# Optimization experiments

Hardware: AMD Instinct MI355X
Metric: run time of the kernel (lower is better)

## Reference

```python
import jax, jax.numpy as jnp
import numpy as np

B, D_IN, N_EXP, D_EXP, TOP_K = 8192, 1024, 8, 1024, 2


def setup_inputs() -> dict:
    key = jax.random.key(0)
    ks = jax.random.split(key, 6)
    s_in = 1.0 / np.sqrt(D_IN)
    s_exp = 1.0 / np.sqrt(D_EXP)
    return {
        "x": jax.random.normal(ks[0], (B, D_IN), jnp.float32),
        "gate_w": jax.random.normal(ks[1], (D_IN, N_EXP), jnp.float32) * s_in,
        "w1": jax.random.normal(ks[2], (N_EXP, D_IN, D_EXP), jnp.float32) * s_in,
        "b1": jax.random.normal(ks[3], (N_EXP, D_EXP), jnp.float32) * 0.01,
        "w2": jax.random.normal(ks[4], (N_EXP, D_EXP, D_EXP), jnp.float32) * s_exp,
        "b2": jax.random.normal(ks[5], (N_EXP, D_EXP), jnp.float32) * 0.01,
    }


def _moe(x, gate_w, w1, b1, w2, b2):
    # Gating: top-k sparse softmax over expert logits.
    gate_logits = x @ gate_w                          # (B, E)
    top_vals, top_idx = jax.lax.top_k(gate_logits, TOP_K)  # (B, K)
    # softmax over only the top-k logits == softmax of -inf-scattered logits
    top_w = jax.nn.softmax(top_vals, axis=-1)          # (B, K)
    gate_weights = jnp.zeros_like(gate_logits).at[
        jnp.arange(x.shape[0])[:, None], top_idx
    ].set(top_w)                                       # (B, E)
    # Dense all-expert MLP (matches torch.stack over experts).
    h = jax.nn.gelu(jnp.einsum("bd,edf->ebf", x, w1) + b1[:, None, :],
                    approximate=False)                 # (E, B, F)
    expert_outs = jnp.einsum("ebf,efg->ebg", h, w2) + b2[:, None, :]  # (E, B, G)
    output = jnp.einsum("be,ebg->bg", gate_weights, expert_outs)      # (B, G)
    return output, gate_weights


def reference(x, gate_w, w1, b1, w2, b2):
    return _moe(x, gate_w, w1, b1, w2, b2)
```

## Files before the change

kernel.cpp:

```cpp
#include <hip/hip_runtime.h>
#include <math.h>
#include <stdint.h>


#define NTOK   8192
#define DIN    1024
#define NEXP   8
#define DEXP   1024
#define MAXROWS 17408
#define MAXTILES 136

typedef __bf16 bf16x8_t __attribute__((ext_vector_type(8)));
typedef float f32x4 __attribute__((ext_vector_type(4)));

__device__ __forceinline__ unsigned short f2bf(float f) {
  union { float f; unsigned int u; } v; v.f = f;
  unsigned int u = v.u;
  u += 0x7fffu + ((u >> 16) & 1u);
  return (unsigned short)(u >> 16);
}

__device__ __forceinline__ float bf2f(unsigned short s) {
  union { unsigned int u; float f; } v; v.u = ((unsigned int)s) << 16;
  return v.f;
}

__device__ __forceinline__ void async16(const void* g, void* l) {
  __builtin_amdgcn_global_load_lds((const __attribute__((address_space(1))) void*)g,
                                   (__attribute__((address_space(3))) void*)l, 16, 0, 0);
}

__device__ __forceinline__ float gelu_fast(float v) {
  float u = v * (1.5957691216057308f + 0.07135481627f * v * v);
  return v * (1.0f / (1.0f + __expf(-u)));
}

__global__ __launch_bounds__(256) void prep_kernel(const float* __restrict__ x,
                                                   const float* __restrict__ gw,
                                                   const float* __restrict__ w1,
                                                   const float* __restrict__ w2,
                                                   unsigned short* __restrict__ xbf,
                                                   unsigned short* __restrict__ w1T,
                                                   unsigned short* __restrict__ w2T,
                                                   float* __restrict__ outGate,
                                                   int* __restrict__ topE,
                                                   float* __restrict__ topW,
                                                   int* __restrict__ rowTok) {
  __shared__ float tile[64][68];
  int b = blockIdx.x;
  int tid = threadIdx.x;
  if (b < 4096) {
    int z = b >> 8;
    const float* src = (z < 8) ? w1 : w2;
    unsigned short* dst = (z < 8) ? w1T : w2T;
    int e = z & 7;
    int idx = b & 255, kt = idx >> 4, nt = idx & 15;
    const float* s = src + (size_t)e * DIN * DEXP + (size_t)kt * 64 * 1024 + nt * 64;
    unsigned short* d = dst + (size_t)e * DIN * DEXP + (size_t)nt * 64 * 1024 + kt * 64;
    int c4 = (tid & 15) * 4, r0 = tid >> 4;
    #pragma unroll
    for (int p = 0; p < 4; ++p) {
      int r = r0 + p * 16;
      *(float4*)&tile[r][c4] = *(const float4*)(s + (size_t)r * 1024 + c4);
    }
    __syncthreads();
    #pragma unroll
    for (int p = 0; p < 4; ++p) {
      int nr = r0 + p * 16;
      ushort4 o;
      o.x = f2bf(tile[c4 + 0][nr]);
      o.y = f2bf(tile[c4 + 1][nr]);
      o.z = f2bf(tile[c4 + 2][nr]);
      o.w = f2bf(tile[c4 + 3][nr]);
      *(ushort4*)(d + (size_t)nr * 1024 + c4) = o;
    }
  } else if (b < 6144) {
    int lane = tid & 63, wv = tid >> 6;
    int t = (b - 4096) * 4 + wv;
    const float4* xr = (const float4*)(x + (size_t)t * 1024);
    ushort4* xo = (ushort4*)(xbf + (size_t)t * 1024);
    double acc[NEXP];
    #pragma unroll
    for (int e = 0; e < NEXP; ++e) acc[e] = 0.0;
    #pragma unroll
    for (int j = 0; j < 4; ++j) {
      int q = lane + 64 * j;
      float4 v = xr[q];
      ushort4 r;
      r.x = f2bf(v.x); r.y = f2bf(v.y); r.z = f2bf(v.z); r.w = f2bf(v.w);
      xo[q] = r;
      float vv[4] = {v.x, v.y, v.z, v.w};
      #pragma unroll
      for (int m = 0; m < 4; ++m) {
        int k = q * 4 + m;
        float4 g0 = *(const float4*)(gw + k * 8);
        float4 g1 = *(const float4*)(gw + k * 8 + 4);
        double xv = (double)vv[m];
        acc[0] += xv * (double)g0.x; acc[1] += xv * (double)g0.y;
        acc[2] += xv * (double)g0.z; acc[3] += xv * (double)g0.w;
        acc[4] += xv * (double)g1.x; acc[5] += xv * (double)g1.y;
        acc[6] += xv * (double)g1.z; acc[7] += xv * (double)g1.w;
      }
    }
    #pragma unroll
    for (int off = 32; off > 0; off >>= 1) {
      #pragma unroll
      for (int e = 0; e < NEXP; ++e) acc[e] += __shfl_xor(acc[e], off);
    }
    if (lane == 0) {
      int e0 = 0; double v0 = acc[0];
      #pragma unroll
      for (int e = 1; e < NEXP; ++e) if (acc[e] > v0) { v0 = acc[e]; e0 = e; }
      int e1 = -1; double v1 = -1e300;
      #pragma unroll
      for (int e = 0; e < NEXP; ++e) if (e != e0 && acc[e] > v1) { v1 = acc[e]; e1 = e; }
      float ex = expf((float)(v1 - v0));
      float inv = 1.0f / (1.0f + ex);
      float w0 = inv, w1v = ex * inv;
      float g8[8];
      #pragma unroll
      for (int e = 0; e < NEXP; ++e) g8[e] = 0.f;
      g8[e0] = w0; g8[e1] = w1v;
      float4* gp = (float4*)(outGate + t * 8);
      gp[0] = *(float4*)&g8[0];
      gp[1] = *(float4*)&g8[4];
      topE[t * 2 + 0] = e0; topE[t * 2 + 1] = e1;
      topW[t * 2 + 0] = w0; topW[t * 2 + 1] = w1v;
    }
  } else {
    int base = (b - 6144) * 1024 + tid * 4;
    int4 m1 = make_int4(-1, -1, -1, -1);
    *(int4*)(rowTok + base) = m1;
  }
}

__global__ __launch_bounds__(1024) void slot_kernel(const int* __restrict__ topE,
                                                    int* __restrict__ topRow,
                                                    int* __restrict__ rowTok,
                                                    int* __restrict__ tileExpert,
                                                    int* __restrict__ tileRowBase) {
  __shared__ int wtot[16][NEXP];
  __shared__ int wbase[16][NEXP];
  __shared__ int soff[NEXP];
  int tid = threadIdx.x, lane = tid & 63, wv = tid >> 6;
  int a0 = tid * 16;
  unsigned long long pk = 0ull;
  int cnt[NEXP];
  #pragma unroll
  for (int e = 0; e < NEXP; ++e) cnt[e] = 0;
  for (int i = 0; i < 16; ++i) {
    int e = topE[a0 + i];
    pk |= (unsigned long long)e << (i * 4);
    cnt[e]++;
  }
  int excl[NEXP];
  #pragma unroll
  for (int e = 0; e < NEXP; ++e) {
    int v = cnt[e], sum = v;
    #pragma unroll
    for (int d = 1; d < 64; d <<= 1) {
      int u = __shfl_up(sum, d);
      if (lane >= d) sum += u;
    }
    excl[e] = sum - v;
    if (lane == 63) wtot[wv][e] = sum;
  }
  __syncthreads();
  if (tid == 0) {
    int counts[NEXP];
    for (int e = 0; e < NEXP; ++e) {
      int s = 0;
      for (int w = 0; w < 16; ++w) { wbase[w][e] = s; s += wtot[w][e]; }
      counts[e] = s;
    }
    int row = 0, tile = 0;
    for (int e = 0; e < NEXP; ++e) {
      soff[e] = row;
      int nt = (counts[e] + 127) >> 7;
      for (int i = 0; i < nt; ++i) { tileExpert[tile] = e; tileRowBase[tile] = row + i * 128; ++tile; }
      row += nt << 7;
    }
    for (; tile < MAXTILES; ++tile) tileExpert[tile] = -1;
  }
  __syncthreads();
  int base[NEXP], run[NEXP];
  #pragma unroll
  for (int e = 0; e < NEXP; ++e) { base[e] = soff[e] + wbase[wv][e] + excl[e]; run[e] = 0; }
  for (int i = 0; i < 16; ++i) {
    int e = (int)((pk >> (i * 4)) & 7ull);
    int row = base[e] + run[e]++;
    rowTok[row] = (a0 + i) >> 1;
    topRow[a0 + i] = row;
  }
}

__global__ __launch_bounds__(256) void gemm1_kernel(const unsigned short* __restrict__ xbf,
                                                    const unsigned short* __restrict__ w1T,
                                                    const float* __restrict__ b1,
                                                    const int* __restrict__ tileExpert,
                                                    const int* __restrict__ tileRowBase,
                                                    const int* __restrict__ rowTok,
                                                    unsigned short* __restrict__ h) {
  int tileId = blockIdx.x;
  int e = tileExpert[tileId];
  if (e < 0) return;
  int rowBase = tileRowBase[tileId];
  int n0 = blockIdx.y * 128;
  __shared__ __align__(16) unsigned short sm[128 * 64 * 2];
  unsigned short* sA = sm;
  unsigned short* sB = sm + 128 * 64;
  int tid = threadIdx.x, lane = tid & 63, wv = tid >> 6;
  int srow = tid >> 3;
  int scolSw = (((tid & 7) ^ ((tid >> 3) & 7)) * 8);
  int tok[4];
  #pragma unroll
  for (int i = 0; i < 4; ++i) {
    int tk = rowTok[rowBase + srow + i * 32];
    tok[i] = tk < 0 ? 0 : tk;
  }
  const unsigned short* Bmat = w1T + (size_t)e * DIN * DEXP;
  int wm = ((tid >> 6) & 1) * 64, wn = (tid >> 7) * 64;
  int rsel = lane & 15, q = lane >> 4;
  int rk = rsel & 7;
  f32x4 acc[4][4] = {};
  for (int kk = 0; kk < DIN; kk += 64) {
    #pragma unroll
    for (int i = 0; i < 4; ++i) {
      int abase = __builtin_amdgcn_readfirstlane((wv * 8 + i * 32) * 128);
      async16(xbf + (size_t)tok[i] * 1024 + kk + scolSw, (char*)sm + abase);
      async16(Bmat + (size_t)(n0 + srow + i * 32) * 1024 + kk + scolSw,
              (char*)sm + abase + 16384);
    }
    __syncthreads();
    #pragma unroll
    for (int ks = 0; ks < 64; ks += 32) {
      int co = (((ks >> 3) + q) ^ rk) * 8;
      bf16x8_t af[4], bfr[4];
      #pragma unroll
      for (int mi = 0; mi < 4; ++mi)
        af[mi] = *(const bf16x8_t*)&sA[(wm + mi * 16 + rsel) * 64 + co];
      #pragma unroll
      for (int ni = 0; ni < 4; ++ni)
        bfr[ni] = *(const bf16x8_t*)&sB[(wn + ni * 16 + rsel) * 64 + co];
      #pragma unroll
      for (int mi = 0; mi < 4; ++mi)
        #pragma unroll
        for (int ni = 0; ni < 4; ++ni)
          acc[mi][ni] = __builtin_amdgcn_mfma_f32_16x16x32_bf16(af[mi], bfr[ni], acc[mi][ni], 0, 0, 0);
    }
    __syncthreads();
  }
  float b1v[4];
  int quad = lane >> 4;
  #pragma unroll
  for (int ni = 0; ni < 4; ++ni) b1v[ni] = b1[e * 1024 + n0 + wn + ni * 16 + rsel];
  #pragma unroll
  for (int mi = 0; mi < 4; ++mi)
    #pragma unroll
    for (int ni = 0; ni < 4; ++ni)
      #pragma unroll
      for (int r = 0; r < 4; ++r) {
        int m = wm + mi * 16 + quad * 4 + r;
        int n = wn + ni * 16 + rsel;
        sm[m * 128 + n] = f2bf(gelu_fast(acc[mi][ni][r] + b1v[ni]));
      }
  __syncthreads();
  #pragma unroll
  for (int i = 0; i < 8; ++i) {
    int idx = i * 2048 + tid * 8;
    int m = idx >> 7, c = idx & 127;
    int g = rowBase + m;
    *(uint4*)(h + (size_t)g * 1024 + n0 + c) = *(const uint4*)&sm[idx];
  }
}

__global__ __launch_bounds__(256) void gemm2_kernel(const unsigned short* __restrict__ h,
                                                    const unsigned short* __restrict__ w2T,
                                                    const float* __restrict__ b2,
                                                    const int* __restrict__ tileExpert,
                                                    const int* __restrict__ tileRowBase,
                                                    unsigned short* __restrict__ y) {
  int tileId = blockIdx.x;
  int e = tileExpert[tileId];
  if (e < 0) return;
  int rowBase = tileRowBase[tileId];
  int n0 = blockIdx.y * 128;
  __shared__ __align__(16) unsigned short sm[128 * 64 * 2];
  unsigned short* sA = sm;
  unsigned short* sB = sm + 128 * 64;
  int tid = threadIdx.x, lane = tid & 63, wv = tid >> 6;
  int srow = tid >> 3;
  int scolSw = (((tid & 7) ^ ((tid >> 3) & 7)) * 8);
  const unsigned short* Bmat = w2T + (size_t)e * DEXP * DEXP;
  int wm = ((tid >> 6) & 1) * 64, wn = (tid >> 7) * 64;
  int rsel = lane & 15, q = lane >> 4;
  int rk = rsel & 7;
  f32x4 acc[4][4] = {};
  for (int kk = 0; kk < DEXP; kk += 64) {
    #pragma unroll
    for (int i = 0; i < 4; ++i) {
      int abase = __builtin_amdgcn_readfirstlane((wv * 8 + i * 32) * 128);
      async16(h + (size_t)(rowBase + srow + i * 32) * 1024 + kk + scolSw, (char*)sm + abase);
      async16(Bmat + (size_t)(n0 + srow + i * 32) * 1024 + kk + scolSw,
              (char*)sm + abase + 16384);
    }
    __syncthreads();
    #pragma unroll
    for (int ks = 0; ks < 64; ks += 32) {
      int co = (((ks >> 3) + q) ^ rk) * 8;
      bf16x8_t af[4], bfr[4];
      #pragma unroll
      for (int mi = 0; mi < 4; ++mi)
        af[mi] = *(const bf16x8_t*)&sA[(wm + mi * 16 + rsel) * 64 + co];
      #pragma unroll
      for (int ni = 0; ni < 4; ++ni)
        bfr[ni] = *(const bf16x8_t*)&sB[(wn + ni * 16 + rsel) * 64 + co];
      #pragma unroll
      for (int mi = 0; mi < 4; ++mi)
        #pragma unroll
        for (int ni = 0; ni < 4; ++ni)
          acc[mi][ni] = __builtin_amdgcn_mfma_f32_16x16x32_bf16(af[mi], bfr[ni], acc[mi][ni], 0, 0, 0);
    }
    __syncthreads();
  }
  float b2v[4];
  int quad = lane >> 4;
  #pragma unroll
  for (int ni = 0; ni < 4; ++ni) b2v[ni] = b2[e * 1024 + n0 + wn + ni * 16 + rsel];
  #pragma unroll
  for (int mi = 0; mi < 4; ++mi)
    #pragma unroll
    for (int ni = 0; ni < 4; ++ni)
      #pragma unroll
      for (int r = 0; r < 4; ++r) {
        int m = wm + mi * 16 + quad * 4 + r;
        int n = wn + ni * 16 + rsel;
        sm[m * 128 + n] = f2bf(acc[mi][ni][r] + b2v[ni]);
      }
  __syncthreads();
  #pragma unroll
  for (int i = 0; i < 8; ++i) {
    int idx = i * 2048 + tid * 8;
    int m = idx >> 7, c = idx & 127;
    int g = rowBase + m;
    *(uint4*)(y + (size_t)g * 1024 + n0 + c) = *(const uint4*)&sm[idx];
  }
}

__global__ __launch_bounds__(256) void combine_kernel(const unsigned short* __restrict__ y,
                                                      const int* __restrict__ topRow,
                                                      const float* __restrict__ topW,
                                                      float* __restrict__ out) {
  int tid = threadIdx.x;
  int wv = tid >> 6, lane = tid & 63;
  int t = blockIdx.x * 4 + wv;
  int r0 = topRow[t * 2 + 0], r1 = topRow[t * 2 + 1];
  float w0 = topW[t * 2 + 0], w1 = topW[t * 2 + 1];
  const unsigned short* p0 = y + (size_t)r0 * 1024 + lane * 16;
  const unsigned short* p1 = y + (size_t)r1 * 1024 + lane * 16;
  float* op = out + (size_t)t * 1024 + lane * 16;
  #pragma unroll
  for (int hh = 0; hh < 2; ++hh) {
    union { uint4 v; unsigned short s[8]; } a, b;
    a.v = *(const uint4*)(p0 + hh * 8);
    b.v = *(const uint4*)(p1 + hh * 8);
    float o[8];
    #pragma unroll
    for (int j = 0; j < 8; ++j)
      o[j] = w0 * bf2f(a.s[j]) + w1 * bf2f(b.s[j]);
    *(float4*)(op + hh * 8) = *(float4*)&o[0];
    *(float4*)(op + hh * 8 + 4) = *(float4*)&o[4];
  }
}

extern "C" void kernel_launch(void* const* d_in, const int* in_sizes, int n_in,
                              void* d_out, int out_size, void* d_ws, size_t ws_size,
                              hipStream_t stream) {
  const float* x  = (const float*)d_in[0];
  const float* gw = (const float*)d_in[1];
  const float* w1 = (const float*)d_in[2];
  const float* b1 = (const float*)d_in[3];
  const float* w2 = (const float*)d_in[4];
  const float* b2 = (const float*)d_in[5];
  float* out = (float*)d_out;

  char* ws = (char*)d_ws;
  int* tileExpert  = (int*)ws;
  int* tileRowBase = tileExpert + MAXTILES;
  int* topE        = tileRowBase + MAXTILES;
  int* topRow      = topE + 16384;
  float* topW      = (float*)(topRow + 16384);
  int* rowTok      = (int*)(ws + (256 << 10));
  unsigned short* xbf  = (unsigned short*)(ws + (512 << 10));
  unsigned short* w1T  = xbf + (size_t)NTOK * DIN;
  unsigned short* w2T  = w1T + (size_t)NEXP * DIN * DEXP;
  unsigned short* hbuf = w2T + (size_t)NEXP * DEXP * DEXP;
  unsigned short* ybuf = hbuf + (size_t)MAXROWS * DEXP;

  prep_kernel<<<4096 + 2048 + 17, 256, 0, stream>>>(x, gw, w1, w2, xbf, w1T, w2T,
                                                    out + (size_t)NTOK * DEXP,
                                                    topE, topW, rowTok);
  slot_kernel<<<1, 1024, 0, stream>>>(topE, topRow, rowTok, tileExpert, tileRowBase);
  gemm1_kernel<<<dim3(MAXTILES, 8), 256, 0, stream>>>(xbf, w1T, b1, tileExpert, tileRowBase,
                                                      rowTok, hbuf);
  gemm2_kernel<<<dim3(MAXTILES, 8), 256, 0, stream>>>(hbuf, w2T, b2, tileExpert, tileRowBase,
                                                      ybuf);
  combine_kernel<<<NTOK / 4, 256, 0, stream>>>(ybuf, topRow, topW, out);
}
```

Before: 330.4 us.

## Load expert weight fragments directly from global into registers, bypass LDS

Both expert GEMMs stop staging the B (weight) tile through shared memory. Each lane now loads its MFMA B fragments straight from global memory into registers before the barrier, which halves LDS traffic and staging per k-step. The cost is that the four waves fetch duplicate weight data from global/L2 instead of sharing one staged copy, and load latency is no longer hidden by the async copies. Separately, the weight transpose in the prep kernel switches to a padded column-major LDS layout with wider 16-byte stores.

```diff
diff --git a/kernel.cpp b/kernel.cpp
--- a/kernel.cpp
+++ b/kernel.cpp
@@ -46,7 +46,7 @@
                                                    int* __restrict__ topE,
                                                    float* __restrict__ topW,
                                                    int* __restrict__ rowTok) {
-  __shared__ float tile[64][68];
+  __shared__ float lds[64 * 65];
   int b = blockIdx.x;
   int tid = threadIdx.x;
   if (b < 4096) {
@@ -61,18 +61,24 @@
     #pragma unroll
     for (int p = 0; p < 4; ++p) {
       int r = r0 + p * 16;
-      *(float4*)&tile[r][c4] = *(const float4*)(s + (size_t)r * 1024 + c4);
+      float4 v = *(const float4*)(s + (size_t)r * 1024 + c4);
+      lds[(c4 + 0) * 65 + r] = v.x;
+      lds[(c4 + 1) * 65 + r] = v.y;
+      lds[(c4 + 2) * 65 + r] = v.z;
+      lds[(c4 + 3) * 65 + r] = v.w;
     }
     __syncthreads();
-    #pragma unroll
-    for (int p = 0; p < 4; ++p) {
-      int nr = r0 + p * 16;
-      ushort4 o;
-      o.x = f2bf(tile[c4 + 0][nr]);
-      o.y = f2bf(tile[c4 + 1][nr]);
-      o.z = f2bf(tile[c4 + 2][nr]);
-      o.w = f2bf(tile[c4 + 3][nr]);
-      *(ushort4*)(d + (size_t)nr * 1024 + c4) = o;
+    int nr = tid >> 2, ksb = (tid & 3) * 16;
+    #pragma unroll
+    for (int m = 0; m < 2; ++m) {
+      unsigned int o[4];
+      #pragma unroll
+      for (int i = 0; i < 4; ++i) {
+        unsigned int lo = f2bf(lds[nr * 65 + ksb + m * 8 + i * 2]);
+        unsigned int hi = f2bf(lds[nr * 65 + ksb + m * 8 + i * 2 + 1]);
+        o[i] = lo | (hi << 16);
+      }
+      *(uint4*)(d + (size_t)nr * 1024 + ksb + m * 8) = *(uint4*)o;
     }
   } else if (b < 6144) {
     int lane = tid & 63, wv = tid >> 6;
@@ -206,9 +212,7 @@
   if (e < 0) return;
   int rowBase = tileRowBase[tileId];
   int n0 = blockIdx.y * 128;
-  __shared__ __align__(16) unsigned short sm[128 * 64 * 2];
-  unsigned short* sA = sm;
-  unsigned short* sB = sm + 128 * 64;
+  __shared__ __align__(16) unsigned short sm[128 * 128];
   int tid = threadIdx.x, lane = tid & 63, wv = tid >> 6;
   int srow = tid >> 3;
   int scolSw = (((tid & 7) ^ ((tid >> 3) & 7)) * 8);
@@ -218,35 +222,39 @@
     int tk = rowTok[rowBase + srow + i * 32];
     tok[i] = tk < 0 ? 0 : tk;
   }
-  const unsigned short* Bmat = w1T + (size_t)e * DIN * DEXP;
   int wm = ((tid >> 6) & 1) * 64, wn = (tid >> 7) * 64;
-  int rsel = lane & 15, q = lane >> 4;
+  int rsel = lane & 15, q = lane >> 4, q8 = q * 8;
   int rk = rsel & 7;
+  const unsigned short* Brow[4];
+  #pragma unroll
+  for (int ni = 0; ni < 4; ++ni)
+    Brow[ni] = w1T + (size_t)e * DIN * DEXP + (size_t)(n0 + wn + ni * 16 + rsel) * 1024 + q8;
   f32x4 acc[4][4] = {};
   for (int kk = 0; kk < DIN; kk += 64) {
     #pragma unroll
     for (int i = 0; i < 4; ++i) {
       int abase = __builtin_amdgcn_readfirstlane((wv * 8 + i * 32) * 128);
       async16(xbf + (size_t)tok[i] * 1024 + kk + scolSw, (char*)sm + abase);
-      async16(Bmat + (size_t)(n0 + srow + i * 32) * 1024 + kk + scolSw,
-              (char*)sm + abase + 16384);
-    }
+    }
+    bf16x8_t bfr[2][4];
+    #pragma unroll
+    for (int ks2 = 0; ks2 < 2; ++ks2)
+      #pragma unroll
+      for (int ni = 0; ni < 4; ++ni)
+        bfr[ks2][ni] = *(const bf16x8_t*)(Brow[ni] + kk + ks2 * 32);
     __syncthreads();
     #pragma unroll
-    for (int ks = 0; ks < 64; ks += 32) {
-      int co = (((ks >> 3) + q) ^ rk) * 8;
-      bf16x8_t af[4], bfr[4];
+    for (int ks2 = 0; ks2 < 2; ++ks2) {
+      int co = (((ks2 * 4) + q) ^ rk) * 8;
+      bf16x8_t af[4];
       #pragma unroll
       for (int mi = 0; mi < 4; ++mi)
-        af[mi] = *(const bf16x8_t*)&sA[(wm + mi * 16 + rsel) * 64 + co];
-      #pragma unroll
-      for (int ni = 0; ni < 4; ++ni)
-        bfr[ni] = *(const bf16x8_t*)&sB[(wn + ni * 16 + rsel) * 64 + co];
+        af[mi] = *(const bf16x8_t*)&sm[(wm + mi * 16 + rsel) * 64 + co];
       #pragma unroll
       for (int mi = 0; mi < 4; ++mi)
         #pragma unroll
         for (int ni = 0; ni < 4; ++ni)
-          acc[mi][ni] = __builtin_amdgcn_mfma_f32_16x16x32_bf16(af[mi], bfr[ni], acc[mi][ni], 0, 0, 0);
+          acc[mi][ni] = __builtin_amdgcn_mfma_f32_16x16x32_bf16(af[mi], bfr[ks2][ni], acc[mi][ni], 0, 0, 0);
     }
     __syncthreads();
   }
@@ -285,41 +293,43 @@
   if (e < 0) return;
   int rowBase = tileRowBase[tileId];
   int n0 = blockIdx.y * 128;
-  __shared__ __align__(16) unsigned short sm[128 * 64 * 2];
-  unsigned short* sA = sm;
-  unsigned short* sB = sm + 128 * 64;
+  __shared__ __align__(16) unsigned short sm[128 * 128];
   int tid = threadIdx.x, lane = tid & 63, wv = tid >> 6;
   int srow = tid >> 3;
   int scolSw = (((tid & 7) ^ ((tid >> 3) & 7)) * 8);
-  const unsigned short* Bmat = w2T + (size_t)e * DEXP * DEXP;
   int wm = ((tid >> 6) & 1) * 64, wn = (tid >> 7) * 64;
-  int rsel = lane & 15, q = lane >> 4;
+  int rsel = lane & 15, q = lane >> 4, q8 = q * 8;
   int rk = rsel & 7;
+  const unsigned short* Brow[4];
+  #pragma unroll
+  for (int ni = 0; ni < 4; ++ni)
+    Brow[ni] = w2T + (size_t)e * DEXP * DEXP + (size_t)(n0 + wn + ni * 16 + rsel) * 1024 + q8;
   f32x4 acc[4][4] = {};
   for (int kk = 0; kk < DEXP; kk += 64) {
     #pragma unroll
     for (int i = 0; i < 4; ++i) {
       int abase = __builtin_amdgcn_readfirstlane((wv * 8 + i * 32) * 128);
       async16(h + (size_t)(rowBase + srow + i * 32) * 1024 + kk + scolSw, (char*)sm + abase);
-      async16(Bmat + (size_t)(n0 + srow + i * 32) * 1024 + kk + scolSw,
-              (char*)sm + abase + 16384);
-    }
+    }
+    bf16x8_t bfr[2][4];
+    #pragma unroll
+    for (int ks2 = 0; ks2 < 2; ++ks2)
+      #pragma unroll
+      for (int ni = 0; ni < 4; ++ni)
+        bfr[ks2][ni] = *(const bf16x8_t*)(Brow[ni] + kk + ks2 * 32);
     __syncthreads();
     #pragma unroll
-    for (int ks = 0; ks < 64; ks += 32) {
-      int co = (((ks >> 3) + q) ^ rk) * 8;
-      bf16x8_t af[4], bfr[4];
+    for (int ks2 = 0; ks2 < 2; ++ks2) {
+      int co = (((ks2 * 4) + q) ^ rk) * 8;
+      bf16x8_t af[4];
       #pragma unroll
       for (int mi = 0; mi < 4; ++mi)
-        af[mi] = *(const bf16x8_t*)&sA[(wm + mi * 16 + rsel) * 64 + co];
-      #pragma unroll
-      for (int ni = 0; ni < 4; ++ni)
-        bfr[ni] = *(const bf16x8_t*)&sB[(wn + ni * 16 + rsel) * 64 + co];
+        af[mi] = *(const bf16x8_t*)&sm[(wm + mi * 16 + rsel) * 64 + co];
       #pragma unroll
       for (int mi = 0; mi < 4; ++mi)
         #pragma unroll
         for (int ni = 0; ni < 4; ++ni)
-          acc[mi][ni] = __builtin_amdgcn_mfma_f32_16x16x32_bf16(af[mi], bfr[ni], acc[mi][ni], 0, 0, 0);
+          acc[mi][ni] = __builtin_amdgcn_mfma_f32_16x16x32_bf16(af[mi], bfr[ks2][ni], acc[mi][ni], 0, 0, 0);
     }
     __syncthreads();
   }
```

After: 420.5 us. 1.27x slower.
